# Kernel optimization log

Hardware: AMD Instinct MI355X
Metric: run time of the kernel (lower is better)

## Reference

```python
import jax, jax.numpy as jnp
import numpy as np

B = 8192          # batch
CIN = 256         # in_channels
COUT = 64         # out_channels
K = 3             # kernel_size
NK = 4            # num_kernels
HIDDEN = int(CIN * 0.25)   # attention hidden = int(in_channels*ratio) = 64
TEMP = 34.0       # attention temperature
KAN_IN = 64 * 4   # base*4 = flattened conv output (COUT*2*2)
GRID_SIZE, SPLINE_ORDER = 5, 3
GMIN, GMAX = -1.0, 1.0
NUM_BASES = GRID_SIZE + SPLINE_ORDER  # 8


def setup_inputs() -> dict:
    key = jax.random.key(0)
    ks = jax.random.split(key, 8)
    s = 0.05
    return {
        "x": jax.random.normal(ks[0], (B, CIN, 4, 4), jnp.float32),
        # dynamic-conv kernel bank [num_kernels, out, in, k, k]
        "weight": jax.random.normal(ks[1], (NK, COUT, CIN, K, K), jnp.float32) * s,
        "bias": jnp.zeros((NK, COUT), jnp.float32),
        # Attention2D: GAP -> fc1 (1x1 conv == linear) -> ReLU -> fc2 -> softmax(/T)
        "fc1_w": jax.random.normal(ks[2], (HIDDEN, CIN), jnp.float32) * s,
        "fc1_b": jnp.zeros((HIDDEN,), jnp.float32),
        "fc2_w": jax.random.normal(ks[3], (NK, HIDDEN), jnp.float32) * s,
        "fc2_b": jnp.zeros((NK,), jnp.float32),
        # KANLinear params (efficient-KAN style)
        "kan_base_w": jax.random.normal(ks[4], (COUT, KAN_IN), jnp.float32) * s,
        "kan_spline_w": jax.random.normal(ks[5], (COUT, KAN_IN, NUM_BASES), jnp.float32) * s,
        "kan_spline_scaler": jnp.ones((COUT, KAN_IN), jnp.float32),
    }


def _bspline_bases(x):
    """Cox-de Boor B-spline bases; x [B, F] -> [B, F, GRID_SIZE+SPLINE_ORDER]."""
    h = (GMAX - GMIN) / GRID_SIZE
    # extended grid, shared across features: length grid_size + 2*order + 1 = 12
    grid = jnp.arange(-SPLINE_ORDER, GRID_SIZE + SPLINE_ORDER + 1, dtype=x.dtype) * h + GMIN
    xe = x[..., None]  # [B, F, 1]
    bases = ((xe >= grid[:-1]) & (xe < grid[1:])).astype(x.dtype)  # order 0
    for k in range(1, SPLINE_ORDER + 1):
        left = (xe - grid[: -(k + 1)]) / (grid[k:-1] - grid[: -(k + 1)]) * bases[..., :-1]
        right = (grid[k + 1:] - xe) / (grid[k + 1:] - grid[1:-k]) * bases[..., 1:]
        bases = left + right
    return bases  # [B, F, 8]


def reference(x, weight, bias, fc1_w, fc1_b, fc2_w, fc2_b,
              kan_base_w, kan_spline_w, kan_spline_scaler):
    b = x.shape[0]
    # --- Attention2D: softmax over kernel bank ---
    pooled = x.mean(axis=(2, 3))                                  # [B, CIN]
    hid = jax.nn.relu(pooled @ fc1_w.T + fc1_b)                   # [B, HIDDEN]
    attn = jax.nn.softmax((hid @ fc2_w.T + fc2_b) / TEMP, axis=-1)  # [B, NK]
    # --- per-sample dynamic conv, fused form ---
    # sum_k a[b,k] * conv(x, W_k) == conv with per-sample aggregated weight
    w_all = weight.reshape(NK * COUT, CIN, K, K)
    y = jax.lax.conv_general_dilated(
        x, w_all, window_strides=(1, 1), padding="VALID",
        dimension_numbers=("NCHW", "OIHW", "NCHW"))                # [B, NK*COUT, 2, 2]
    y = y.reshape(b, NK, COUT, y.shape[-2], y.shape[-1])
    conv_out = jnp.einsum("bk,bkohw->bohw", attn, y)
    conv_out = conv_out + (attn @ bias)[:, :, None, None]          # aggregated bias
    # --- KANLinear on flattened conv output ---
    feat = conv_out.reshape(b, -1)                                 # [B, 256]
    base_out = jax.nn.silu(feat) @ kan_base_w.T                    # [B, COUT]
    bases = _bspline_bases(feat)                                   # [B, 256, 8]
    spline_out = jnp.einsum("big,oig->bo", bases,
                            kan_spline_w * kan_spline_scaler[..., None])
    return base_out + spline_out                                   # [B, COUT]
```

## Files before the change

kernel.cpp:

```cpp
#include <hip/hip_runtime.h>

#define BT   8192
#define MS   16
#define XBUF (MS * 656)

typedef _Float16 half8  __attribute__((ext_vector_type(8)));
typedef _Float16 half4v __attribute__((ext_vector_type(4)));
typedef float    floatx4  __attribute__((ext_vector_type(4)));
typedef float    floatx16 __attribute__((ext_vector_type(16)));

__global__ __launch_bounds__(256) void prep_kernel(
    const float* __restrict__ weight, const float* __restrict__ base_w,
    const float* __restrict__ spline_w, const float* __restrict__ scaler,
    const float* __restrict__ fc1_w,
    _Float16* __restrict__ W3, _Float16* __restrict__ Wk3,
    _Float16* __restrict__ Wf3)
{
    const int bb = blockIdx.x;
    const int tid = threadIdx.x;
    if (bb < 256) {
        const int n = bb;
        const int c = tid;
        const float* src = weight + ((size_t)n * 256 + c) * 9;
        const int cc = c >> 5, ci = c & 31;
        #pragma unroll
        for (int ij = 0; ij < 9; ++ij) {
            W3[((size_t)(cc * 9 + ij) * 256 + n) * 32 + ci] = (_Float16)src[ij];
        }
    } else if (bb < 328) {
        const int st = bb - 256;
        #pragma unroll
        for (int u = 0; u < 8; ++u) {
            const int idx = u * 256 + tid;
            const int n = idx >> 5, kk = idx & 31;
            const int k = st * 32 + kk;
            float v;
            if (k < 256) {
                v = base_w[n * 256 + k];
            } else {
                const int r = k - 256;
                const int i = r >> 3, g = r & 7;
                v = spline_w[((size_t)n * 256 + i) * 8 + g] * scaler[n * 256 + i];
            }
            Wk3[(size_t)st * 2048 + idx] = (_Float16)v;
        }
    } else {
        const int st2 = bb - 328;
        #pragma unroll
        for (int u = 0; u < 8; ++u) {
            const int idx = u * 256 + tid;
            const int n = idx >> 5, kk = idx & 31;
            Wf3[(size_t)st2 * 2048 + idx] = (_Float16)fc1_w[n * 256 + st2 * 32 + kk];
        }
    }
}

__device__ __forceinline__ void bases8c(float xv, _Float16* dst) {
    const float t = (xv + 2.2f) * 2.5f;
    const float ft = floorf(t);
    const int idx = (int)ft;
    const float u = t - ft, v = 1.f - u;
    const float u2 = u * u, v2 = v * v;
    const float c3 = u2 * u * (1.f / 6.f);
    const float c2 = (1.f / 6.f) + 0.5f * (u + u2 - u2 * u);
    const float c1 = (1.f / 6.f) + 0.5f * (v + v2 - v2 * v);
    const float c0 = v2 * v * (1.f / 6.f);
    half8 hb;
    #pragma unroll
    for (int tt = 0; tt < 8; ++tt) {
        const int d = idx - tt;
        float b = 0.f;
        b = (d == 0) ? c3 : b;
        b = (d == 1) ? c2 : b;
        b = (d == 2) ? c1 : b;
        b = (d == 3) ? c0 : b;
        hb[tt] = (_Float16)b;
    }
    *(half8*)dst = hb;
}

__global__ __launch_bounds__(512, 4) void fused_kernel(
    const float* __restrict__ x, const _Float16* __restrict__ W3,
    const _Float16* __restrict__ Wk3, const _Float16* __restrict__ Wf3,
    const float* __restrict__ bias, const float* __restrict__ fc1_b,
    const float* __restrict__ fc2_w, const float* __restrict__ fc2_b,
    float* __restrict__ out)
{
    __shared__ __align__(16) char smem[MS * 2312 * 2];
    __shared__ float hid_lds[MS * 68];
    __shared__ float attn_s[MS][4];

    _Float16* Xs  = (_Float16*)smem;
    _Float16* Pl  = (_Float16*)(smem + 2 * XBUF * 2);
    _Float16* Act = (_Float16*)smem;

    const int tid = threadIdx.x;
    const int wv = tid >> 6, lane = tid & 63;
    const int nl = lane & 15, q = lane >> 4;
    const int cg = wv & 3, kh = wv >> 2;
    const int b0i = blockIdx.x * MS;

    const int posr = nl & 3;
    const int aLane = (nl >> 2) * 656 + ((posr >> 1) * 4 + (posr & 1)) * 40 + q * 8
                    + kh * 5248;
    const int lbW = (cg * 16 + nl) * 32 + q * 8;

    const int s_ = tid >> 5, cch = tid & 31;
    const float* xg = x + ((size_t)(b0i + s_) * 256 + cch) * 16;

    floatx4 acc[2][4];
    #pragma unroll
    for (int r2 = 0; r2 < 2; ++r2)
        #pragma unroll
        for (int kb = 0; kb < 4; ++kb)
            acc[r2][kb] = floatx4{0.f, 0.f, 0.f, 0.f};

    half8 b0[4], b1[4];
    #pragma unroll
    for (int kb = 0; kb < 4; ++kb)
        b0[kb] = *(const half8*)(W3 + kb * 2048 + lbW);
    #pragma unroll
    for (int kb = 0; kb < 4; ++kb)
        b1[kb] = *(const half8*)(W3 + 8192 + kb * 2048 + lbW);

    floatx16 r = *(const floatx16*)xg;
    {
        _Float16* xd = &Xs[s_ * 656 + cch];
        #pragma unroll
        for (int p = 0; p < 16; ++p) xd[p * 40] = (_Float16)r[p];
        float sm = 0.f;
        #pragma unroll
        for (int p = 0; p < 16; ++p) sm += r[p];
        Pl[s_ * 264 + cch] = (_Float16)(sm * (1.0f / 16.0f));
    }
    r = *(const floatx16*)(xg + 512);
    __syncthreads();

    #pragma unroll 1
    for (int cc = 0; cc < 8; ++cc) {
        const int cur = cc & 1;
        if (cc < 7) {
            _Float16* xd = &Xs[(cur ^ 1) * XBUF + s_ * 656 + cch];
            #pragma unroll
            for (int p = 0; p < 16; ++p) xd[p * 40] = (_Float16)r[p];
            float sm = 0.f;
            #pragma unroll
            for (int p = 0; p < 16; ++p) sm += r[p];
            Pl[s_ * 264 + (cc + 1) * 32 + cch] = (_Float16)(sm * (1.0f / 16.0f));
        }
        if (cc < 6) r = *(const floatx16*)(xg + (cc + 2) * 512);

        const _Float16* wst = W3 + (size_t)cc * 9 * 8192 + lbW;
        const _Float16* xb = &Xs[cur * XBUF + aLane];

        const int p0tab[9] = {0, 1, 2, 4, 5, 6, 8, 9, 10};

        #pragma unroll
        for (int ij = 0; ij < 9; ++ij) {
            const _Float16* wnx = (cc * 9 + ij + 2 < 72)
                                ? (wst + (size_t)(ij + 2) * 8192)
                                : (W3 + lbW);
            half8 b2[4];
            #pragma unroll
            for (int kb = 0; kb < 4; ++kb)
                b2[kb] = *(const half8*)(wnx + kb * 2048);

            const int p0 = p0tab[ij];
            const half8 aF0 = *(const half8*)&xb[p0 * 40];
            const half8 aF1 = *(const half8*)&xb[2624 + p0 * 40];
            #pragma unroll
            for (int kb = 0; kb < 4; ++kb)
                acc[0][kb] = __builtin_amdgcn_mfma_f32_16x16x32_f16(aF0, b0[kb], acc[0][kb], 0, 0, 0);
            #pragma unroll
            for (int kb = 0; kb < 4; ++kb)
                acc[1][kb] = __builtin_amdgcn_mfma_f32_16x16x32_f16(aF1, b0[kb], acc[1][kb], 0, 0, 0);
            #pragma unroll
            for (int kb = 0; kb < 4; ++kb) { b0[kb] = b1[kb]; b1[kb] = b2[kb]; }
        }
        __syncthreads();
    }

    if (kh == 0) {
        floatx4 a1 = floatx4{0.f, 0.f, 0.f, 0.f};
        const _Float16* wfb = Wf3 + ((cg * 16 + nl) * 32 + q * 8);
        const _Float16* pb = &Pl[nl * 264 + q * 8];
        #pragma unroll
        for (int st = 0; st < 8; ++st) {
            const half8 aF = *(const half8*)(pb + st * 32);
            const half8 bF = *(const half8*)(wfb + st * 2048);
            a1 = __builtin_amdgcn_mfma_f32_16x16x32_f16(aF, bF, a1, 0, 0, 0);
        }
        const int h = cg * 16 + nl;
        const float fb = fc1_b[h];
        #pragma unroll
        for (int reg = 0; reg < 4; ++reg)
            hid_lds[(q * 4 + reg) * 68 + h] = fmaxf(a1[reg] + fb, 0.f);
    }
    __syncthreads();

    if (wv == 0) {
        const int s = lane >> 2, kb = lane & 3;
        float l = fc2_b[kb];
        #pragma unroll 8
        for (int h = 0; h < 64; ++h) l += hid_lds[s * 68 + h] * fc2_w[kb * 64 + h];
        float m = fmaxf(l, __shfl_xor(l, 1));
        m = fmaxf(m, __shfl_xor(m, 2));
        const float e = __expf((l - m) * (1.0f / 34.0f));
        float sm = e + __shfl_xor(e, 1);
        sm += __shfl_xor(sm, 2);
        attn_s[s][kb] = e / sm;
    }
    __syncthreads();

    const int o = cg * 16 + nl;
    {
        const float bb0 = bias[o], bb1 = bias[64 + o], bb2 = bias[128 + o], bb3 = bias[192 + o];
        #pragma unroll
        for (int r2 = 0; r2 < 2; ++r2) {
            const int s = (kh * 2 + r2) * 4 + q;
            const float a0 = attn_s[s][0], a1 = attn_s[s][1],
                        a2 = attn_s[s][2], a3 = attn_s[s][3];
            const float badd = a0 * bb0 + a1 * bb1 + a2 * bb2 + a3 * bb3;
            float f[4];
            #pragma unroll
            for (int e = 0; e < 4; ++e) {
                f[e] = a0 * acc[r2][0][e] + a1 * acc[r2][1][e]
                     + a2 * acc[r2][2][e] + a3 * acc[r2][3][e] + badd;
            }
            half4v sv;
            #pragma unroll
            for (int e = 0; e < 4; ++e) {
                const float ex = __expf(-f[e]);
                sv[e] = (_Float16)(f[e] * __builtin_amdgcn_rcpf(1.f + ex));
            }
            *(half4v*)&Act[s * 2312 + o * 4] = sv;
            #pragma unroll
            for (int e = 0; e < 4; ++e)
                bases8c(f[e], &Act[s * 2312 + 256 + (o * 4 + e) * 8]);
        }
    }
    __syncthreads();

    {
        floatx4 a2 = floatx4{0.f, 0.f, 0.f, 0.f};
        const _Float16* wkb = Wk3 + ((size_t)(cg * 16 + nl) * 32 + q * 8);
        const _Float16* ab = &Act[nl * 2312 + q * 8];
        const int st0 = kh * 36;
        half8 kb0 = *(const half8*)(wkb + (size_t)st0 * 2048);
        half8 kb1 = *(const half8*)(wkb + (size_t)(st0 + 1) * 2048);
        #pragma unroll 4
        for (int i = 0; i < 36; ++i) {
            half8 kb2;
            if (i < 34) kb2 = *(const half8*)(wkb + (size_t)(st0 + i + 2) * 2048);
            const half8 aF = *(const half8*)(ab + (st0 + i) * 32);
            a2 = __builtin_amdgcn_mfma_f32_16x16x32_f16(aF, kb0, a2, 0, 0, 0);
            kb0 = kb1; kb1 = kb2;
        }
        if (kh == 1) *(floatx4*)&hid_lds[cg * 256 + lane * 4] = a2;
        __syncthreads();
        if (kh == 0) {
            const floatx4 p = *(const floatx4*)&hid_lds[cg * 256 + lane * 4];
            a2 = a2 + p;
            #pragma unroll
            for (int reg = 0; reg < 4; ++reg)
                out[(size_t)(b0i + q * 4 + reg) * 64 + cg * 16 + nl] = a2[reg];
        }
    }
}

extern "C" void kernel_launch(void* const* d_in, const int* in_sizes, int n_in,
                              void* d_out, int out_size, void* d_ws, size_t ws_size,
                              hipStream_t stream) {
    const float* x          = (const float*)d_in[0];
    const float* weight     = (const float*)d_in[1];
    const float* bias       = (const float*)d_in[2];
    const float* fc1_w      = (const float*)d_in[3];
    const float* fc1_b      = (const float*)d_in[4];
    const float* fc2_w      = (const float*)d_in[5];
    const float* fc2_b      = (const float*)d_in[6];
    const float* kan_base_w = (const float*)d_in[7];
    const float* kan_spline = (const float*)d_in[8];
    const float* kan_scaler = (const float*)d_in[9];
    float* out = (float*)d_out;

    _Float16* W3  = (_Float16*)d_ws;
    _Float16* Wk3 = W3 + (size_t)72 * 8192;
    _Float16* Wf3 = Wk3 + (size_t)72 * 2048;

    prep_kernel<<<336, 256, 0, stream>>>(weight, kan_base_w, kan_spline,
                                         kan_scaler, fc1_w, W3, Wk3, Wf3);
    fused_kernel<<<BT / MS, 512, 0, stream>>>(x, W3, Wk3, Wf3, bias, fc1_b,
                                              fc2_w, fc2_b, out);
}
```

Before: 276.8 us.

## Halve samples per block and repartition conv MFMA tiles across four waves

Cuts the block tile from 16 to 8 samples with 256 threads, so each wave now owns a 64-wide slice of the 256 conv output channels (kernel-major) instead of a per-kernel channel group. The attention-weighted sum over the four kernels therefore moves to a new LDS transpose step: raw accumulators are written out, then re-read per sample to build the aggregated feature, SiLU and spline bases. The KAN GEMM now runs all 72 K-steps per wave instead of splitting across two wave halves with a cross-wave reduction. This doubles grid size for better occupancy and load balance. In exchange, half the MFMA rows are wasted (8 samples in 16-row tiles), more weight is re-read per sample, and an extra LDS round-trip is added.

```diff
diff --git a/kernel.cpp b/kernel.cpp
--- a/kernel.cpp
+++ b/kernel.cpp
@@ -1,7 +1,7 @@
 #include <hip/hip_runtime.h>
 
 #define BT   8192
-#define MS   16
+#define MS   8
 #define XBUF (MS * 656)
 
 typedef _Float16 half8  __attribute__((ext_vector_type(8)));
@@ -79,7 +79,7 @@
     *(half8*)dst = hb;
 }
 
-__global__ __launch_bounds__(512, 4) void fused_kernel(
+__global__ __launch_bounds__(256, 4) void fused_kernel(
     const float* __restrict__ x, const _Float16* __restrict__ W3,
     const _Float16* __restrict__ Wk3, const _Float16* __restrict__ Wf3,
     const float* __restrict__ bias, const float* __restrict__ fc1_b,
@@ -97,31 +97,29 @@
     const int tid = threadIdx.x;
     const int wv = tid >> 6, lane = tid & 63;
     const int nl = lane & 15, q = lane >> 4;
-    const int cg = wv & 3, kh = wv >> 2;
     const int b0i = blockIdx.x * MS;
 
     const int posr = nl & 3;
-    const int aLane = (nl >> 2) * 656 + ((posr >> 1) * 4 + (posr & 1)) * 40 + q * 8
-                    + kh * 5248;
-    const int lbW = (cg * 16 + nl) * 32 + q * 8;
+    const int aLane = (nl >> 2) * 656 + ((posr >> 1) * 4 + (posr & 1)) * 40 + q * 8;
+    const int lbW = ((wv * 4) * 16 + nl) * 32 + q * 8;
 
     const int s_ = tid >> 5, cch = tid & 31;
     const float* xg = x + ((size_t)(b0i + s_) * 256 + cch) * 16;
 
     floatx4 acc[2][4];
     #pragma unroll
-    for (int r2 = 0; r2 < 2; ++r2)
-        #pragma unroll
-        for (int kb = 0; kb < 4; ++kb)
-            acc[r2][kb] = floatx4{0.f, 0.f, 0.f, 0.f};
+    for (int rt = 0; rt < 2; ++rt)
+        #pragma unroll
+        for (int t = 0; t < 4; ++t)
+            acc[rt][t] = floatx4{0.f, 0.f, 0.f, 0.f};
 
     half8 b0[4], b1[4];
     #pragma unroll
-    for (int kb = 0; kb < 4; ++kb)
-        b0[kb] = *(const half8*)(W3 + kb * 2048 + lbW);
-    #pragma unroll
-    for (int kb = 0; kb < 4; ++kb)
-        b1[kb] = *(const half8*)(W3 + 8192 + kb * 2048 + lbW);
+    for (int t = 0; t < 4; ++t)
+        b0[t] = *(const half8*)(W3 + lbW + t * 512);
+    #pragma unroll
+    for (int t = 0; t < 4; ++t)
+        b1[t] = *(const half8*)(W3 + 8192 + lbW + t * 512);
 
     floatx16 r = *(const floatx16*)xg;
     {
@@ -162,43 +160,45 @@
                                 : (W3 + lbW);
             half8 b2[4];
             #pragma unroll
-            for (int kb = 0; kb < 4; ++kb)
-                b2[kb] = *(const half8*)(wnx + kb * 2048);
+            for (int t = 0; t < 4; ++t)
+                b2[t] = *(const half8*)(wnx + t * 512);
 
             const int p0 = p0tab[ij];
             const half8 aF0 = *(const half8*)&xb[p0 * 40];
             const half8 aF1 = *(const half8*)&xb[2624 + p0 * 40];
             #pragma unroll
-            for (int kb = 0; kb < 4; ++kb)
-                acc[0][kb] = __builtin_amdgcn_mfma_f32_16x16x32_f16(aF0, b0[kb], acc[0][kb], 0, 0, 0);
-            #pragma unroll
-            for (int kb = 0; kb < 4; ++kb)
-                acc[1][kb] = __builtin_amdgcn_mfma_f32_16x16x32_f16(aF1, b0[kb], acc[1][kb], 0, 0, 0);
-            #pragma unroll
-            for (int kb = 0; kb < 4; ++kb) { b0[kb] = b1[kb]; b1[kb] = b2[kb]; }
+            for (int t = 0; t < 4; ++t)
+                acc[0][t] = __builtin_amdgcn_mfma_f32_16x16x32_f16(aF0, b0[t], acc[0][t], 0, 0, 0);
+            #pragma unroll
+            for (int t = 0; t < 4; ++t)
+                acc[1][t] = __builtin_amdgcn_mfma_f32_16x16x32_f16(aF1, b0[t], acc[1][t], 0, 0, 0);
+            #pragma unroll
+            for (int t = 0; t < 4; ++t) { b0[t] = b1[t]; b1[t] = b2[t]; }
         }
         __syncthreads();
     }
 
-    if (kh == 0) {
+    {
         floatx4 a1 = floatx4{0.f, 0.f, 0.f, 0.f};
-        const _Float16* wfb = Wf3 + ((cg * 16 + nl) * 32 + q * 8);
-        const _Float16* pb = &Pl[nl * 264 + q * 8];
+        const _Float16* wfb = Wf3 + ((wv * 16 + nl) * 32 + q * 8);
+        const _Float16* pb = &Pl[(nl & 7) * 264 + q * 8];
         #pragma unroll
         for (int st = 0; st < 8; ++st) {
             const half8 aF = *(const half8*)(pb + st * 32);
             const half8 bF = *(const half8*)(wfb + st * 2048);
             a1 = __builtin_amdgcn_mfma_f32_16x16x32_f16(aF, bF, a1, 0, 0, 0);
         }
-        const int h = cg * 16 + nl;
-        const float fb = fc1_b[h];
-        #pragma unroll
-        for (int reg = 0; reg < 4; ++reg)
-            hid_lds[(q * 4 + reg) * 68 + h] = fmaxf(a1[reg] + fb, 0.f);
-    }
-    __syncthreads();
-
-    if (wv == 0) {
+        if (q < 2) {
+            const int h = wv * 16 + nl;
+            const float fb = fc1_b[h];
+            #pragma unroll
+            for (int reg = 0; reg < 4; ++reg)
+                hid_lds[(q * 4 + reg) * 68 + h] = fmaxf(a1[reg] + fb, 0.f);
+        }
+    }
+    __syncthreads();
+
+    if (wv == 0 && lane < 32) {
         const int s = lane >> 2, kb = lane & 3;
         float l = fc2_b[kb];
         #pragma unroll 8
@@ -210,60 +210,64 @@
         sm += __shfl_xor(sm, 2);
         attn_s[s][kb] = e / sm;
     }
-    __syncthreads();
-
-    const int o = cg * 16 + nl;
-    {
-        const float bb0 = bias[o], bb1 = bias[64 + o], bb2 = bias[128 + o], bb3 = bias[192 + o];
-        #pragma unroll
-        for (int r2 = 0; r2 < 2; ++r2) {
-            const int s = (kh * 2 + r2) * 4 + q;
-            const float a0 = attn_s[s][0], a1 = attn_s[s][1],
-                        a2 = attn_s[s][2], a3 = attn_s[s][3];
-            const float badd = a0 * bb0 + a1 * bb1 + a2 * bb2 + a3 * bb3;
-            float f[4];
+    #pragma unroll
+    for (int rt = 0; rt < 2; ++rt) {
+        const int s = rt * 4 + q;
+        #pragma unroll
+        for (int t = 0; t < 4; ++t) {
             #pragma unroll
             for (int e = 0; e < 4; ++e) {
-                f[e] = a0 * acc[r2][0][e] + a1 * acc[r2][1][e]
-                     + a2 * acc[r2][2][e] + a3 * acc[r2][3][e] + badd;
+                const int f = (t * 16 + nl) * 4 + e;
+                float* fp = (float*)&Act[s * 2312 + 256 + f * 8];
+                fp[wv] = acc[rt][t][e];
             }
-            half4v sv;
-            #pragma unroll
-            for (int e = 0; e < 4; ++e) {
-                const float ex = __expf(-f[e]);
-                sv[e] = (_Float16)(f[e] * __builtin_amdgcn_rcpf(1.f + ex));
-            }
-            *(half4v*)&Act[s * 2312 + o * 4] = sv;
-            #pragma unroll
-            for (int e = 0; e < 4; ++e)
-                bases8c(f[e], &Act[s * 2312 + 256 + (o * 4 + e) * 8]);
-        }
+        }
+    }
+    __syncthreads();
+
+    {
+        const int sl = lane >> 5, fl = lane & 31;
+        const int s = wv * 2 + sl;
+        const float a0 = attn_s[s][0], a1 = attn_s[s][1],
+                    a2 = attn_s[s][2], a3 = attn_s[s][3];
+        const int o0 = fl * 2, f0 = fl * 8;
+        const float badd0 = a0 * bias[o0] + a1 * bias[64 + o0]
+                          + a2 * bias[128 + o0] + a3 * bias[192 + o0];
+        const float badd1 = a0 * bias[o0 + 1] + a1 * bias[64 + o0 + 1]
+                          + a2 * bias[128 + o0 + 1] + a3 * bias[192 + o0 + 1];
+        half8 sv;
+        #pragma unroll
+        for (int u = 0; u < 8; ++u) {
+            float* fp = (float*)&Act[s * 2312 + 256 + (f0 + u) * 8];
+            const floatx4 P = *(const floatx4*)fp;
+            const float fv = a0 * P[0] + a1 * P[1] + a2 * P[2] + a3 * P[3]
+                           + ((u < 4) ? badd0 : badd1);
+            const float ex = __expf(-fv);
+            sv[u] = (_Float16)(fv * __builtin_amdgcn_rcpf(1.f + ex));
+            bases8c(fv, (_Float16*)fp);
+        }
+        *(half8*)&Act[s * 2312 + o0 * 4] = sv;
     }
     __syncthreads();
 
     {
         floatx4 a2 = floatx4{0.f, 0.f, 0.f, 0.f};
-        const _Float16* wkb = Wk3 + ((size_t)(cg * 16 + nl) * 32 + q * 8);
-        const _Float16* ab = &Act[nl * 2312 + q * 8];
-        const int st0 = kh * 36;
-        half8 kb0 = *(const half8*)(wkb + (size_t)st0 * 2048);
-        half8 kb1 = *(const half8*)(wkb + (size_t)(st0 + 1) * 2048);
+        const _Float16* wkb = Wk3 + ((size_t)(wv * 16 + nl) * 32 + q * 8);
+        const _Float16* ab = &Act[(nl & 7) * 2312 + q * 8];
+        half8 kb0 = *(const half8*)(wkb);
+        half8 kb1 = *(const half8*)(wkb + 2048);
         #pragma unroll 4
-        for (int i = 0; i < 36; ++i) {
+        for (int i = 0; i < 72; ++i) {
             half8 kb2;
-            if (i < 34) kb2 = *(const half8*)(wkb + (size_t)(st0 + i + 2) * 2048);
-            const half8 aF = *(const half8*)(ab + (st0 + i) * 32);
+            if (i < 70) kb2 = *(const half8*)(wkb + (size_t)(i + 2) * 2048);
+            const half8 aF = *(const half8*)(ab + i * 32);
             a2 = __builtin_amdgcn_mfma_f32_16x16x32_f16(aF, kb0, a2, 0, 0, 0);
             kb0 = kb1; kb1 = kb2;
         }
-        if (kh == 1) *(floatx4*)&hid_lds[cg * 256 + lane * 4] = a2;
-        __syncthreads();
-        if (kh == 0) {
-            const floatx4 p = *(const floatx4*)&hid_lds[cg * 256 + lane * 4];
-            a2 = a2 + p;
+        if (q < 2) {
             #pragma unroll
             for (int reg = 0; reg < 4; ++reg)
-                out[(size_t)(b0i + q * 4 + reg) * 64 + cg * 16 + nl] = a2[reg];
+                out[(size_t)(b0i + q * 4 + reg) * 64 + wv * 16 + nl] = a2[reg];
         }
     }
 }
@@ -289,6 +293,6 @@
 
     prep_kernel<<<336, 256, 0, stream>>>(weight, kan_base_w, kan_spline,
                                          kan_scaler, fc1_w, W3, Wk3, Wf3);
-    fused_kernel<<<BT / MS, 512, 0, stream>>>(x, W3, Wk3, Wf3, bias, fc1_b,
+    fused_kernel<<<BT / MS, 256, 0, stream>>>(x, W3, Wk3, Wf3, bias, fc1_b,
                                               fc2_w, fc2_b, out);
 }
```

Result: slower. 284.7 us (+2.9%).
